# Performance work log

Measured on AMD Instinct MI355X. Metric: run time of the kernel, lower is better.

The kernel has to match this reference:

```python
import jax, jax.numpy as jnp
import numpy as np

D_MODEL = 768
EXPAND = 2
D_INNER = EXPAND * D_MODEL  # 1536
D_STATE = 16
D_CONV = 4
DT_RANK = (D_MODEL + 15) // 16  # 48, ceil(d_model/16)
BATCH, SEQ = 8, 2048
EPS = 1e-12


def _silu(x):
    return x * jax.nn.sigmoid(x)


def _mamba(x, in_w, conv_w, conv_b, xproj_w, dt_w, dt_b, A_log, D_skip, out_w):
    # x: (B, L, d_model)
    B, L, _ = x.shape
    xz = x @ in_w.T                      # (B, L, 2*d_inner)
    u, z = jnp.split(xz, 2, axis=-1)     # each (B, L, d_inner)
    # causal depthwise conv1d, kernel D_CONV, left-pad D_CONV-1
    pad = jnp.pad(u, ((0, 0), (D_CONV - 1, 0), (0, 0)))
    uc = conv_b + sum(pad[:, k:k + L, :] * conv_w[:, k] for k in range(D_CONV))
    uc = _silu(uc)                       # (B, L, d_inner)
    x_dbl = uc @ xproj_w.T               # (B, L, dt_rank + 2*d_state)
    dt, Bm, Cm = jnp.split(x_dbl, [DT_RANK, DT_RANK + D_STATE], axis=-1)
    dt = jax.nn.softplus(dt @ dt_w.T + dt_b)  # (B, L, d_inner)
    A = -jnp.exp(A_log)                  # (d_inner, d_state)

    def step(h, t):
        dt_t, B_t, C_t, u_t = t          # (B,di), (B,N), (B,N), (B,di)
        dA = jnp.exp(dt_t[:, :, None] * A)               # (B, di, N)
        h = dA * h + (dt_t * u_t)[:, :, None] * B_t[:, None, :]
        y = jnp.einsum('bdn,bn->bd', h, C_t)
        return h, y

    xs = (dt.swapaxes(0, 1), Bm.swapaxes(0, 1), Cm.swapaxes(0, 1), uc.swapaxes(0, 1))
    h0 = jnp.zeros((B, D_INNER, D_STATE), x.dtype)
    _, ys = jax.lax.scan(step, h0, xs)   # ys: (L, B, d_inner)
    y = ys.swapaxes(0, 1) + uc * D_skip
    return (y * _silu(z)) @ out_w.T      # (B, L, d_model)


def _mamba_params(key):
    ks = jax.random.split(key, 8)
    return dict(
        in_w=jax.random.normal(ks[0], (2 * D_INNER, D_MODEL), jnp.float32) * 0.02,
        conv_w=jax.random.normal(ks[1], (D_INNER, D_CONV), jnp.float32) * 0.2,
        conv_b=jnp.zeros((D_INNER,), jnp.float32),
        xproj_w=jax.random.normal(ks[2], (DT_RANK + 2 * D_STATE, D_INNER), jnp.float32) * 0.02,
        dt_w=jax.random.normal(ks[3], (D_INNER, DT_RANK), jnp.float32) * 0.02,
        dt_b=jax.random.normal(ks[4], (D_INNER,), jnp.float32) * 0.02,
        A_log=jnp.log(jnp.tile(jnp.arange(1, D_STATE + 1, dtype=jnp.float32), (D_INNER, 1))),
        D_skip=jnp.ones((D_INNER,), jnp.float32),
        out_w=jax.random.normal(ks[5], (D_MODEL, D_INNER), jnp.float32) * 0.02,
    )


def setup_inputs() -> dict:
    key = jax.random.key(0)
    k0, k1, k2 = jax.random.split(key, 3)
    inp = {'hidden_states': jax.random.normal(k0, (BATCH, SEQ, D_MODEL), jnp.float32)}
    for pref, k in (('f_', k1), ('b_', k2)):
        for name, v in _mamba_params(k).items():
            inp[pref + name] = v
    inp['ln_g'] = jnp.ones((D_MODEL,), jnp.float32)
    inp['ln_b'] = jnp.zeros((D_MODEL,), jnp.float32)
    return inp


def reference(hidden_states,
              f_in_w, f_conv_w, f_conv_b, f_xproj_w, f_dt_w, f_dt_b, f_A_log, f_D_skip, f_out_w,
              b_in_w, b_conv_w, b_conv_b, b_xproj_w, b_dt_w, b_dt_b, b_A_log, b_D_skip, b_out_w,
              ln_g, ln_b):
    hf = _mamba(hidden_states, f_in_w, f_conv_w, f_conv_b, f_xproj_w, f_dt_w, f_dt_b,
                f_A_log, f_D_skip, f_out_w)
    hb = jnp.flip(_mamba(jnp.flip(hidden_states, 1), b_in_w, b_conv_w, b_conv_b, b_xproj_w,
                         b_dt_w, b_dt_b, b_A_log, b_D_skip, b_out_w), 1)
    h = hf + hb + hidden_states          # dropout is identity at eval
    mu = h.mean(-1, keepdims=True)
    var = ((h - mu) ** 2).mean(-1, keepdims=True)
    return (h - mu) / jnp.sqrt(var + EPS) * ln_g + ln_b
```

## Files before the change

### kernel.cpp

```cpp
#include <hip/hip_runtime.h>
#include <math.h>

#define D_MODEL 768
#define D_INNER 1536
#define D_STATE 16
#define DCONV 4
#define DT_RANK 48
#define BATCH 8
#define SEQ 2048
#define NROWS (BATCH * SEQ)
#define NXZ (2 * D_INNER)
#define NDBC (DT_RANK + 2 * D_STATE)

#define NCHUNK 16
#define CL (SEQ / NCHUNK)
#define NCH (BATCH * D_INNER)
#define DBLKS (D_INNER / 256)

#define LOG2E 1.4426950408889634f
#define LN2   0.6931471805599453f

typedef __attribute__((ext_vector_type(8))) short bh8;
typedef __attribute__((ext_vector_type(4))) float f4;
typedef __attribute__((ext_vector_type(8))) unsigned short us8;

__device__ __forceinline__ float bf2f(unsigned short u) {
    return __uint_as_float(((unsigned int)u) << 16);
}
__device__ __forceinline__ unsigned short f2bf(float f) {
    unsigned int x = __float_as_uint(f);
    return (unsigned short)((x + 0x7fffu + ((x >> 16) & 1u)) >> 16);
}
__device__ __forceinline__ float fsigm(float x) {
    return __builtin_amdgcn_rcpf(1.f + __builtin_amdgcn_exp2f(-x * LOG2E));
}

#define GLL16(gp, lp) __builtin_amdgcn_global_load_lds( \
    (const __attribute__((address_space(1))) void*)(gp), \
    (__attribute__((address_space(3))) void*)(lp), 16, 0, 0)

template <int TC_BF, int ACC, int ACT>
__global__ __launch_bounds__(256) void gemm_mfma(
    const unsigned short* __restrict__ A, int lda,
    const unsigned short* __restrict__ W, int ldw,
    const float* __restrict__ bias,
    void* __restrict__ Cv, int ldc, int K)
{
    __shared__ unsigned short As[128 * 32];
    __shared__ unsigned short Bs[128 * 32];
    const int tid = threadIdx.x;
    const int w = tid >> 6;
    const int l = tid & 63;
    const int wr = w >> 1, wc = w & 1;
    const int tm0 = blockIdx.y * 128;
    const int tn0 = blockIdx.x * 128;

    const int srow = (w << 4) + (l >> 2);
    const int scol = (l & 3) * 8;
    unsigned short* ldsA0 = &As[(w << 4) * 32];
    unsigned short* ldsA1 = &As[(64 + (w << 4)) * 32];
    unsigned short* ldsB0 = &Bs[(w << 4) * 32];
    unsigned short* ldsB1 = &Bs[(64 + (w << 4)) * 32];
    const unsigned short* gA0 = A + (size_t)(tm0 + srow) * lda + scol;
    const unsigned short* gA1 = A + (size_t)(tm0 + 64 + srow) * lda + scol;
    const unsigned short* gB0 = W + (size_t)(tn0 + srow) * ldw + scol;
    const unsigned short* gB1 = W + (size_t)(tn0 + 64 + srow) * ldw + scol;

    const int aoff = ((wr << 6) + (l & 15)) * 32 + ((l >> 4) << 3);
    const int boff = ((wc << 6) + (l & 15)) * 32 + ((l >> 4) << 3);

    f4 acc[4][4];
#pragma unroll
    for (int i = 0; i < 4; ++i)
#pragma unroll
        for (int j = 0; j < 4; ++j) acc[i][j] = 0.f;

    for (int k0 = 0; k0 < K; k0 += 32) {
        GLL16(gA0 + k0, ldsA0);
        GLL16(gA1 + k0, ldsA1);
        GLL16(gB0 + k0, ldsB0);
        GLL16(gB1 + k0, ldsB1);
        __syncthreads();
        bh8 af[4], bf[4];
#pragma unroll
        for (int mi = 0; mi < 4; ++mi) af[mi] = *(const bh8*)&As[aoff + mi * 512];
#pragma unroll
        for (int ni = 0; ni < 4; ++ni) bf[ni] = *(const bh8*)&Bs[boff + ni * 512];
#pragma unroll
        for (int mi = 0; mi < 4; ++mi)
#pragma unroll
            for (int ni = 0; ni < 4; ++ni)
                acc[mi][ni] = __builtin_amdgcn_mfma_f32_16x16x32_bf16(
                    af[mi], bf[ni], acc[mi][ni], 0, 0, 0);
        __syncthreads();
    }

    const int crow0 = tm0 + (wr << 6) + ((l >> 4) << 2);
    const int ccol0 = tn0 + (wc << 6) + (l & 15);
#pragma unroll
    for (int mi = 0; mi < 4; ++mi)
#pragma unroll
        for (int ni = 0; ni < 4; ++ni)
#pragma unroll
            for (int r = 0; r < 4; ++r) {
                const int n = ccol0 + ni * 16;
                const size_t idx = (size_t)(crow0 + mi * 16 + r) * ldc + n;
                float v = acc[mi][ni][r];
                if (ACT == 1) {
                    v += bias[n];
                    if (v <= 20.f)
                        v = __builtin_amdgcn_logf(1.f + __builtin_amdgcn_exp2f(v * LOG2E)) * LN2;
                }
                if (TC_BF) {
                    ((unsigned short*)Cv)[idx] = f2bf(v);
                } else {
                    float* C = (float*)Cv;
                    C[idx] = ACC ? (C[idx] + v) : v;
                }
            }
}

__global__ __launch_bounds__(256) void gemm_mfma_xp(
    const unsigned short* __restrict__ A, int lda,
    const unsigned short* __restrict__ Wp,
    float* __restrict__ dtBC, unsigned short* __restrict__ dtR, int K)
{
    __shared__ unsigned short As[128 * 32];
    __shared__ unsigned short Bs[128 * 32];
    const int tid = threadIdx.x;
    const int w = tid >> 6;
    const int l = tid & 63;
    const int wr = w >> 1, wc = w & 1;
    const int tm0 = blockIdx.y * 128;

    const int srow = (w << 4) + (l >> 2);
    const int scol = (l & 3) * 8;
    unsigned short* ldsA0 = &As[(w << 4) * 32];
    unsigned short* ldsA1 = &As[(64 + (w << 4)) * 32];
    unsigned short* ldsB0 = &Bs[(w << 4) * 32];
    unsigned short* ldsB1 = &Bs[(64 + (w << 4)) * 32];
    const unsigned short* gA0 = A + (size_t)(tm0 + srow) * lda + scol;
    const unsigned short* gA1 = A + (size_t)(tm0 + 64 + srow) * lda + scol;
    const unsigned short* gB0 = Wp + (size_t)srow * lda + scol;
    const unsigned short* gB1 = Wp + (size_t)(64 + srow) * lda + scol;

    const int aoff = ((wr << 6) + (l & 15)) * 32 + ((l >> 4) << 3);
    const int boff = ((wc << 6) + (l & 15)) * 32 + ((l >> 4) << 3);

    f4 acc[4][4];
#pragma unroll
    for (int i = 0; i < 4; ++i)
#pragma unroll
        for (int j = 0; j < 4; ++j) acc[i][j] = 0.f;

    for (int k0 = 0; k0 < K; k0 += 32) {
        GLL16(gA0 + k0, ldsA0);
        GLL16(gA1 + k0, ldsA1);
        GLL16(gB0 + k0, ldsB0);
        GLL16(gB1 + k0, ldsB1);
        __syncthreads();
        bh8 af[4], bf[4];
#pragma unroll
        for (int mi = 0; mi < 4; ++mi) af[mi] = *(const bh8*)&As[aoff + mi * 512];
#pragma unroll
        for (int ni = 0; ni < 4; ++ni) bf[ni] = *(const bh8*)&Bs[boff + ni * 512];
#pragma unroll
        for (int mi = 0; mi < 4; ++mi)
#pragma unroll
            for (int ni = 0; ni < 4; ++ni)
                acc[mi][ni] = __builtin_amdgcn_mfma_f32_16x16x32_bf16(
                    af[mi], bf[ni], acc[mi][ni], 0, 0, 0);
        __syncthreads();
    }

    const int crow0 = tm0 + (wr << 6) + ((l >> 4) << 2);
    const int ccol0 = (wc << 6) + (l & 15);
#pragma unroll
    for (int mi = 0; mi < 4; ++mi)
#pragma unroll
        for (int ni = 0; ni < 4; ++ni) {
            const int n = ccol0 + ni * 16;
            if (n >= 80) continue;
#pragma unroll
            for (int r = 0; r < 4; ++r) {
                const int m = crow0 + mi * 16 + r;
                const float v = acc[mi][ni][r];
                dtBC[(size_t)m * NDBC + n] = v;
                if (n < 64) dtR[(size_t)m * 64 + n] = f2bf(v);
            }
        }
}

__global__ __launch_bounds__(256) void cast_f32_bf16(
    const float* __restrict__ in, unsigned short* __restrict__ out, int n4)
{
    const int i = blockIdx.x * 256 + threadIdx.x;
    if (i >= n4) return;
    const float4 v = ((const float4*)in)[i];
    ushort4 o;
    o.x = f2bf(v.x); o.y = f2bf(v.y); o.z = f2bf(v.z); o.w = f2bf(v.w);
    ((ushort4*)out)[i] = o;
}

__global__ __launch_bounds__(256) void cast_dtw(
    const float* __restrict__ in, unsigned short* __restrict__ out)
{
    const int i = blockIdx.x * 256 + threadIdx.x;
    if (i >= D_INNER * 64) return;
    const int d = i >> 6, k = i & 63;
    out[i] = (k < DT_RANK) ? f2bf(in[d * DT_RANK + k]) : (unsigned short)0;
}

template <int DIR>
__global__ __launch_bounds__(256) void conv_silu8(
    const unsigned short* __restrict__ xz, const float* __restrict__ conv_w,
    const float* __restrict__ conv_b, unsigned short* __restrict__ uc)
{
    const int idx = blockIdx.x * 256 + threadIdx.x;
    const int row = idx / 192;
    const int dp  = (idx - row * 192) * 8;
    const int l = row & (SEQ - 1);

    f4 cw[8];
#pragma unroll
    for (int i = 0; i < 8; ++i)
        cw[i] = *(const f4*)&conv_w[(dp + i) * 4];

    float acc[8];
    {
        const f4 b0 = *(const f4*)&conv_b[dp];
        const f4 b1 = *(const f4*)&conv_b[dp + 4];
#pragma unroll
        for (int i = 0; i < 4; ++i) { acc[i] = b0[i]; acc[4 + i] = b1[i]; }
    }

#pragma unroll
    for (int j = 0; j < 4; ++j) {
        const int ll = DIR ? (l + j) : (l - j);
        if (ll >= 0 && ll < SEQ) {
            const us8 v = *(const us8*)&xz[((long)row + (ll - l)) * NXZ + dp];
#pragma unroll
            for (int i = 0; i < 8; ++i)
                acc[i] = fmaf(bf2f(v[i]), cw[i][3 - j], acc[i]);
        }
    }
    us8 o;
#pragma unroll
    for (int i = 0; i < 8; ++i)
        o[i] = f2bf(acc[i] * fsigm(acc[i]));
    *(us8*)&uc[(size_t)row * D_INNER + dp] = o;
}

template <int DIR>
__global__ __launch_bounds__(256) void scan1_d(
    const float* __restrict__ dtBC, const unsigned short* __restrict__ uc,
    const float* __restrict__ A_log, const unsigned short* __restrict__ xz,
    float* __restrict__ Fb, float* __restrict__ Sd)
{
    __shared__ float bs[CL][20];
    const int tid = threadIdx.x;
    const int c    = blockIdx.x / (DBLKS * BATCH);
    const int rem  = blockIdx.x % (DBLKS * BATCH);
    const int b    = rem / DBLKS;
    const int dblk = rem % DBLKS;
    const int d = dblk * 256 + tid;
    const long l0 = DIR ? (SEQ - 1 - c * CL) : (c * CL);

    {
        const int rk = tid >> 1, half = tid & 1;
        const long l = DIR ? (l0 - rk) : (l0 + rk);
        const float* src = &dtBC[((size_t)b * SEQ + l) * NDBC + DT_RANK + half * 8];
        *(f4*)&bs[rk][half * 8]     = *(const f4*)src;
        *(f4*)&bs[rk][half * 8 + 4] = *(const f4*)(src + 4);
    }
    __syncthreads();

    float A2[16];
#pragma unroll
    for (int n = 0; n < 16; ++n)
        A2[n] = -expf(A_log[d * D_STATE + n]) * LOG2E;

    const unsigned short* pdt = xz + (size_t)b * SEQ * NXZ + d;
    const unsigned short* pu  = uc + (size_t)b * SEQ * D_INNER + d;

    float h[16];
#pragma unroll
    for (int n = 0; n < 16; ++n) h[n] = 0.f;
    float sdt = 0.f;

    float dt8a[8], u8a[8], dt8b[8], u8b[8];
    auto LOAD = [&](float* dt8, float* u8, int k0) {
#pragma unroll
        for (int j = 0; j < 8; ++j) {
            const long l = DIR ? (l0 - (k0 + j)) : (l0 + (k0 + j));
            dt8[j] = bf2f(pdt[l * NXZ]);
            u8[j]  = bf2f(pu[l * D_INNER]);
        }
    };
    auto COMP = [&](const float* dt8, const float* u8, int k0) {
#pragma unroll
        for (int j = 0; j < 8; ++j) {
            const float dt = dt8[j];
            const float dtu = dt * u8[j];
            sdt += dt;
            const int k = k0 + j;
#pragma unroll
            for (int q = 0; q < 4; ++q) {
                const f4 Bq = *(const f4*)&bs[k][q * 4];
#pragma unroll
                for (int e = 0; e < 4; ++e) {
                    const int n = q * 4 + e;
                    const float dA = __builtin_amdgcn_exp2f(dt * A2[n]);
                    h[n] = fmaf(dA, h[n], dtu * Bq[e]);
                }
            }
        }
    };
    LOAD(dt8a, u8a, 0);
    for (int k0 = 0; k0 < CL; k0 += 16) {
        LOAD(dt8b, u8b, k0 + 8);
        COMP(dt8a, u8a, k0);
        if (k0 + 16 < CL) LOAD(dt8a, u8a, k0 + 16);
        COMP(dt8b, u8b, k0 + 8);
    }

    const int ch = b * D_INNER + d;
    float* fdst = Fb + ((size_t)c * NCH + ch) * 16;
#pragma unroll
    for (int n = 0; n < 16; ++n) fdst[n] = h[n];
    Sd[(size_t)c * NCH + ch] = sdt;
}

__global__ __launch_bounds__(256) void scan_comb(
    float* __restrict__ Fb, const float* __restrict__ Sd,
    const float* __restrict__ A_log)
{
    const int i = blockIdx.x * 256 + threadIdx.x;
    const int ch = i >> 4, n = i & 15;
    const int d = ch % D_INNER;
    const float A2 = -expf(A_log[d * D_STATE + n]) * LOG2E;
    float h = Fb[i];
    for (int cc = 1; cc < NCHUNK - 1; ++cc) {
        const float P = __builtin_amdgcn_exp2f(A2 * Sd[(size_t)cc * NCH + ch]);
        h = fmaf(P, h, Fb[(size_t)cc * (NCH * 16) + i]);
        Fb[(size_t)cc * (NCH * 16) + i] = h;
    }
}

template <int DIR>
__global__ __launch_bounds__(256) void scan2_d(
    const float* __restrict__ dtBC, const unsigned short* __restrict__ uc,
    const float* __restrict__ A_log, const float* __restrict__ D_skip,
    unsigned short* __restrict__ xz, const float* __restrict__ Fb)
{
    __shared__ float bs[CL][36];
    const int tid = threadIdx.x;
    const int c    = blockIdx.x / (DBLKS * BATCH);
    const int rem  = blockIdx.x % (DBLKS * BATCH);
    const int b    = rem / DBLKS;
    const int dblk = rem % DBLKS;
    const int d = dblk * 256 + tid;
    const long l0 = DIR ? (SEQ - 1 - c * CL) : (c * CL);

    {
        const int rk = tid >> 1, half = tid & 1;
        const long l = DIR ? (l0 - rk) : (l0 + rk);
        const float* src = &dtBC[((size_t)b * SEQ + l) * NDBC + DT_RANK + half * 16];
        *(f4*)&bs[rk][half * 16]      = *(const f4*)src;
        *(f4*)&bs[rk][half * 16 + 4]  = *(const f4*)(src + 4);
        *(f4*)&bs[rk][half * 16 + 8]  = *(const f4*)(src + 8);
        *(f4*)&bs[rk][half * 16 + 12] = *(const f4*)(src + 12);
    }
    __syncthreads();

    float A2[16];
#pragma unroll
    for (int n = 0; n < 16; ++n)
        A2[n] = -expf(A_log[d * D_STATE + n]) * LOG2E;
    const float Dv = D_skip[d];

    const unsigned short* pdt = xz + (size_t)b * SEQ * NXZ + d;
    const unsigned short* pz  = pdt + D_INNER;
    const unsigned short* pu  = uc + (size_t)b * SEQ * D_INNER + d;
    unsigned short* pout = xz + (size_t)b * SEQ * NXZ + d;

    const int ch = b * D_INNER + d;
    float h[16];
    if (c == 0) {
#pragma unroll
        for (int n = 0; n < 16; ++n) h[n] = 0.f;
    } else {
        const float* hsrc = Fb + ((size_t)(c - 1) * NCH + ch) * 16;
#pragma unroll
        for (int n = 0; n < 16; ++n) h[n] = hsrc[n];
    }

    float dt8a[8], u8a[8], z8a[8], dt8b[8], u8b[8], z8b[8];
    auto LOAD = [&](float* dt8, float* u8, float* z8, int k0) {
#pragma unroll
        for (int j = 0; j < 8; ++j) {
            const long l = DIR ? (l0 - (k0 + j)) : (l0 + (k0 + j));
            dt8[j] = bf2f(pdt[l * NXZ]);
            u8[j]  = bf2f(pu[l * D_INNER]);
            z8[j]  = bf2f(pz[l * NXZ]);
        }
    };
    auto COMP = [&](const float* dt8, const float* u8, const float* z8, int k0) {
#pragma unroll
        for (int j = 0; j < 8; ++j) {
            const float dt = dt8[j];
            const float dtu = dt * u8[j];
            float ya[4];
            ya[0] = u8[j] * Dv; ya[1] = 0.f; ya[2] = 0.f; ya[3] = 0.f;
            const int k = k0 + j;
#pragma unroll
            for (int q = 0; q < 4; ++q) {
                const f4 Bq = *(const f4*)&bs[k][q * 4];
                const f4 Cq = *(const f4*)&bs[k][16 + q * 4];
#pragma unroll
                for (int e = 0; e < 4; ++e) {
                    const int n = q * 4 + e;
                    const float dA = __builtin_amdgcn_exp2f(dt * A2[n]);
                    h[n] = fmaf(dA, h[n], dtu * Bq[e]);
                    ya[e] = fmaf(h[n], Cq[e], ya[e]);
                }
            }
            const float y = (ya[0] + ya[1]) + (ya[2] + ya[3]);
            const float zv = z8[j];
            const long l = DIR ? (l0 - k) : (l0 + k);
            pout[l * NXZ] = f2bf(y * (zv * fsigm(zv)));
        }
    };
    LOAD(dt8a, u8a, z8a, 0);
    for (int k0 = 0; k0 < CL; k0 += 16) {
        LOAD(dt8b, u8b, z8b, k0 + 8);
        COMP(dt8a, u8a, z8a, k0);
        if (k0 + 16 < CL) LOAD(dt8a, u8a, z8a, k0 + 16);
        COMP(dt8b, u8b, z8b, k0 + 8);
    }
}

__global__ __launch_bounds__(256) void fuse_ln(
    float* __restrict__ out, const float* __restrict__ x,
    const float* __restrict__ g, const float* __restrict__ bta)
{
    const int row = blockIdx.x;
    const size_t base = (size_t)row * D_MODEL;
    float vals[3];
    float s = 0.f, s2 = 0.f;
#pragma unroll
    for (int i = 0; i < 3; ++i) {
        const int c = threadIdx.x + i * 256;
        const float v = out[base + c] + x[base + c];
        vals[i] = v;
        s += v;
        s2 += v * v;
    }
#pragma unroll
    for (int o = 32; o >= 1; o >>= 1) {
        s  += __shfl_xor(s, o, 64);
        s2 += __shfl_xor(s2, o, 64);
    }
    __shared__ float ls[4], ls2[4];
    const int wid = threadIdx.x >> 6;
    if ((threadIdx.x & 63) == 0) { ls[wid] = s; ls2[wid] = s2; }
    __syncthreads();
    s  = ls[0] + ls[1] + ls[2] + ls[3];
    s2 = ls2[0] + ls2[1] + ls2[2] + ls2[3];
    const float mu  = s * (1.f / D_MODEL);
    const float var = s2 * (1.f / D_MODEL) - mu * mu;
    const float inv = 1.f / sqrtf(var + 1e-12f);
#pragma unroll
    for (int i = 0; i < 3; ++i) {
        const int c = threadIdx.x + i * 256;
        out[base + c] = (vals[i] - mu) * inv * g[c] + bta[c];
    }
}

extern "C" void kernel_launch(void* const* d_in, const int* in_sizes, int n_in,
                              void* d_out, int out_size, void* d_ws, size_t ws_size,
                              hipStream_t stream)
{
    const float* x = (const float*)d_in[0];
    const float* ln_g = (const float*)d_in[19];
    const float* ln_b = (const float*)d_in[20];

    float* dtBC = (float*)d_ws;
    unsigned short* xz  = (unsigned short*)(dtBC + (size_t)NROWS * NDBC);
    unsigned short* uc  = xz + (size_t)NROWS * NXZ;
    unsigned short* xbf = uc + (size_t)NROWS * D_INNER;
    unsigned short* wbf_in  = xbf + (size_t)NROWS * D_MODEL;
    unsigned short* wbf_out = wbf_in + (size_t)NXZ * D_MODEL;
    unsigned short* wbf_xp  = wbf_out + (size_t)D_MODEL * D_INNER;
    unsigned short* dtw_pad = wbf_xp + (size_t)128 * D_INNER;
    unsigned short* dtR     = dtw_pad + (size_t)D_INNER * 64;
    float* Fb = (float*)(dtR + (size_t)NROWS * 64);
    float* Sd = Fb + (size_t)(NCHUNK - 1) * NCH * 16;
    const size_t needed = ((size_t)NROWS * NDBC) * 4
        + ((size_t)NROWS * NXZ + (size_t)NROWS * D_INNER + (size_t)NROWS * D_MODEL
           + (size_t)NXZ * D_MODEL + (size_t)D_MODEL * D_INNER
           + (size_t)128 * D_INNER + (size_t)D_INNER * 64 + (size_t)NROWS * 64) * 2
        + (size_t)(NCHUNK - 1) * NCH * 16 * 4
        + (size_t)(NCHUNK - 1) * NCH * 4;
    if (ws_size < needed) return;

    float* outp = (float*)d_out;

    cast_f32_bf16<<<(NROWS * D_MODEL / 4 + 255) / 256, 256, 0, stream>>>(
        x, xbf, NROWS * D_MODEL / 4);

    for (int dir = 0; dir < 2; ++dir) {
        const float* in_w    = (const float*)d_in[1 + dir * 9 + 0];
        const float* conv_w  = (const float*)d_in[1 + dir * 9 + 1];
        const float* conv_b  = (const float*)d_in[1 + dir * 9 + 2];
        const float* xproj_w = (const float*)d_in[1 + dir * 9 + 3];
        const float* dt_w    = (const float*)d_in[1 + dir * 9 + 4];
        const float* dt_b    = (const float*)d_in[1 + dir * 9 + 5];
        const float* A_log   = (const float*)d_in[1 + dir * 9 + 6];
        const float* D_skip  = (const float*)d_in[1 + dir * 9 + 7];
        const float* out_w   = (const float*)d_in[1 + dir * 9 + 8];

        cast_f32_bf16<<<(NXZ * D_MODEL / 4 + 255) / 256, 256, 0, stream>>>(
            in_w, wbf_in, NXZ * D_MODEL / 4);
        cast_f32_bf16<<<(D_MODEL * D_INNER / 4 + 255) / 256, 256, 0, stream>>>(
            out_w, wbf_out, D_MODEL * D_INNER / 4);
        cast_f32_bf16<<<(NDBC * D_INNER / 4 + 255) / 256, 256, 0, stream>>>(
            xproj_w, wbf_xp, NDBC * D_INNER / 4);
        cast_dtw<<<(D_INNER * 64 + 255) / 256, 256, 0, stream>>>(dt_w, dtw_pad);

        gemm_mfma<1, 0, 0><<<dim3(NXZ / 128, NROWS / 128), 256, 0, stream>>>(
            xbf, D_MODEL, wbf_in, D_MODEL, nullptr, xz, NXZ, D_MODEL);

        if (dir == 0)
            conv_silu8<0><<<NROWS * 192 / 256, 256, 0, stream>>>(
                xz, conv_w, conv_b, uc);
        else
            conv_silu8<1><<<NROWS * 192 / 256, 256, 0, stream>>>(
                xz, conv_w, conv_b, uc);

        gemm_mfma_xp<<<dim3(1, NROWS / 128), 256, 0, stream>>>(
            uc, D_INNER, wbf_xp, dtBC, dtR, D_INNER);

        gemm_mfma<1, 0, 1><<<dim3(D_INNER / 128, NROWS / 128), 256, 0, stream>>>(
            dtR, 64, dtw_pad, 64, dt_b, xz, NXZ, 64);

        if (dir == 0) {
            scan1_d<0><<<(NCHUNK - 1) * DBLKS * BATCH, 256, 0, stream>>>(
                dtBC, uc, A_log, xz, Fb, Sd);
            scan_comb<<<NCH * 16 / 256, 256, 0, stream>>>(Fb, Sd, A_log);
            scan2_d<0><<<NCHUNK * DBLKS * BATCH, 256, 0, stream>>>(
                dtBC, uc, A_log, D_skip, xz, Fb);
        } else {
            scan1_d<1><<<(NCHUNK - 1) * DBLKS * BATCH, 256, 0, stream>>>(
                dtBC, uc, A_log, xz, Fb, Sd);
            scan_comb<<<NCH * 16 / 256, 256, 0, stream>>>(Fb, Sd, A_log);
            scan2_d<1><<<NCHUNK * DBLKS * BATCH, 256, 0, stream>>>(
                dtBC, uc, A_log, D_skip, xz, Fb);
        }

        if (dir == 0)
            gemm_mfma<0, 0, 0><<<dim3(D_MODEL / 128, NROWS / 128), 256, 0, stream>>>(
                xz, NXZ, wbf_out, D_INNER, nullptr, outp, D_MODEL, D_INNER);
        else
            gemm_mfma<0, 1, 0><<<dim3(D_MODEL / 128, NROWS / 128), 256, 0, stream>>>(
                xz, NXZ, wbf_out, D_INNER, nullptr, outp, D_MODEL, D_INNER);
    }

    fuse_ln<<<NROWS, 256, 0, stream>>>(outp, x, ln_g, ln_b);
}
```

Before: 987.4 us.

## Split-K the x_proj GEMM with partial-sum reduction and add XCD block swizzle

The x_proj GEMM previously ran only 128 blocks, each looping over the full K=1536, which underfills the GPU. It now splits K into four segments across blockIdx.x, giving 512 blocks, and writes fp32 partial sums. A new reduction kernel adds them and emits dtBC and the bf16 dtR. An XCD-aware block-index swizzle is also added to all MFMA GEMMs to improve L2 locality. The cost is an extra kernel launch and extra partial-sum traffic to global memory.

```diff
diff --git a/kernel.cpp b/kernel.cpp
--- a/kernel.cpp
+++ b/kernel.cpp
@@ -16,6 +16,8 @@
 #define CL (SEQ / NCHUNK)
 #define NCH (BATCH * D_INNER)
 #define DBLKS (D_INNER / 256)
+#define KSEG (D_INNER / 4)
+#define NP ((size_t)NROWS * NDBC)
 
 #define LOG2E 1.4426950408889634f
 #define LN2   0.6931471805599453f
@@ -38,6 +40,14 @@
 #define GLL16(gp, lp) __builtin_amdgcn_global_load_lds( \
     (const __attribute__((address_space(1))) void*)(gp), \
     (__attribute__((address_space(3))) void*)(lp), 16, 0, 0)
+
+__device__ __forceinline__ void xcd_swizzle(int& bx, int& by) {
+    const int nwg = gridDim.x * gridDim.y;
+    const int wid = blockIdx.y * gridDim.x + blockIdx.x;
+    const int work = (wid & 7) * (nwg >> 3) + (wid >> 3);
+    bx = work % gridDim.x;
+    by = work / gridDim.x;
+}
 
 template <int TC_BF, int ACC, int ACT>
 __global__ __launch_bounds__(256) void gemm_mfma(
@@ -48,12 +58,14 @@
 {
     __shared__ unsigned short As[128 * 32];
     __shared__ unsigned short Bs[128 * 32];
+    int bx, by;
+    xcd_swizzle(bx, by);
     const int tid = threadIdx.x;
     const int w = tid >> 6;
     const int l = tid & 63;
     const int wr = w >> 1, wc = w & 1;
-    const int tm0 = blockIdx.y * 128;
-    const int tn0 = blockIdx.x * 128;
+    const int tm0 = by * 128;
+    const int tn0 = bx * 128;
 
     const int srow = (w << 4) + (l >> 2);
     const int scol = (l & 3) * 8;
@@ -123,15 +135,18 @@
 __global__ __launch_bounds__(256) void gemm_mfma_xp(
     const unsigned short* __restrict__ A, int lda,
     const unsigned short* __restrict__ Wp,
-    float* __restrict__ dtBC, unsigned short* __restrict__ dtR, int K)
+    float* __restrict__ Pp)
 {
     __shared__ unsigned short As[128 * 32];
     __shared__ unsigned short Bs[128 * 32];
+    int bx, by;
+    xcd_swizzle(bx, by);
     const int tid = threadIdx.x;
     const int w = tid >> 6;
     const int l = tid & 63;
     const int wr = w >> 1, wc = w & 1;
-    const int tm0 = blockIdx.y * 128;
+    const int tm0 = by * 128;
+    const int kbeg = bx * KSEG;
 
     const int srow = (w << 4) + (l >> 2);
     const int scol = (l & 3) * 8;
@@ -153,7 +168,7 @@
 #pragma unroll
         for (int j = 0; j < 4; ++j) acc[i][j] = 0.f;
 
-    for (int k0 = 0; k0 < K; k0 += 32) {
+    for (int k0 = kbeg; k0 < kbeg + KSEG; k0 += 32) {
         GLL16(gA0 + k0, ldsA0);
         GLL16(gA1 + k0, ldsA1);
         GLL16(gB0 + k0, ldsB0);
@@ -175,6 +190,7 @@
 
     const int crow0 = tm0 + (wr << 6) + ((l >> 4) << 2);
     const int ccol0 = (wc << 6) + (l & 15);
+    float* pdst = Pp + (size_t)bx * NP;
 #pragma unroll
     for (int mi = 0; mi < 4; ++mi)
 #pragma unroll
@@ -184,11 +200,23 @@
 #pragma unroll
             for (int r = 0; r < 4; ++r) {
                 const int m = crow0 + mi * 16 + r;
-                const float v = acc[mi][ni][r];
-                dtBC[(size_t)m * NDBC + n] = v;
-                if (n < 64) dtR[(size_t)m * 64 + n] = f2bf(v);
+                pdst[(size_t)m * NDBC + n] = acc[mi][ni][r];
             }
         }
+}
+
+__global__ __launch_bounds__(256) void xp_reduce(
+    const float* __restrict__ Pp, float* __restrict__ dtBC,
+    unsigned short* __restrict__ dtR)
+{
+    const size_t i = (size_t)blockIdx.x * 256 + threadIdx.x;
+    const float s = (Pp[i] + Pp[i + NP]) + (Pp[i + 2 * NP] + Pp[i + 3 * NP]);
+    dtBC[i] = s;
+    const int n = (int)(i % NDBC);
+    if (n < 64) {
+        const size_t m = i / NDBC;
+        dtR[m * 64 + n] = f2bf(s);
+    }
 }
 
 __global__ __launch_bounds__(256) void cast_f32_bf16(
@@ -496,12 +524,14 @@
     unsigned short* dtR     = dtw_pad + (size_t)D_INNER * 64;
     float* Fb = (float*)(dtR + (size_t)NROWS * 64);
     float* Sd = Fb + (size_t)(NCHUNK - 1) * NCH * 16;
+    float* Pp = Sd + (size_t)(NCHUNK - 1) * NCH;
     const size_t needed = ((size_t)NROWS * NDBC) * 4
         + ((size_t)NROWS * NXZ + (size_t)NROWS * D_INNER + (size_t)NROWS * D_MODEL
            + (size_t)NXZ * D_MODEL + (size_t)D_MODEL * D_INNER
            + (size_t)128 * D_INNER + (size_t)D_INNER * 64 + (size_t)NROWS * 64) * 2
         + (size_t)(NCHUNK - 1) * NCH * 16 * 4
-        + (size_t)(NCHUNK - 1) * NCH * 4;
+        + (size_t)(NCHUNK - 1) * NCH * 4
+        + 4 * NP * 4;
     if (ws_size < needed) return;
 
     float* outp = (float*)d_out;
@@ -538,8 +568,9 @@
             conv_silu8<1><<<NROWS * 192 / 256, 256, 0, stream>>>(
                 xz, conv_w, conv_b, uc);
 
-        gemm_mfma_xp<<<dim3(1, NROWS / 128), 256, 0, stream>>>(
-            uc, D_INNER, wbf_xp, dtBC, dtR, D_INNER);
+        gemm_mfma_xp<<<dim3(4, NROWS / 128), 256, 0, stream>>>(
+            uc, D_INNER, wbf_xp, Pp);
+        xp_reduce<<<(int)(NP / 256), 256, 0, stream>>>(Pp, dtBC, dtR);
 
         gemm_mfma<1, 0, 1><<<dim3(D_INNER / 128, NROWS / 128), 256, 0, stream>>>(
             dtR, 64, dtw_pad, 64, dt_b, xz, NXZ, 64);
```

After: 951.7 us. 3.6% less time.
